# Kernel tuning notes

Measured on AMD Instinct MI355X. Metric: run time of the kernel, lower is better.

The kernel has to match this reference:

```python
import jax, jax.numpy as jnp
import numpy as np

N = 50000      # nodes
E = 800000     # edges (avg degree 16)
DIN = 128
DOUT = 128
L = 8          # num GCN2Conv layers
ALPHA = 0.1
THETA = 0.5


def setup_inputs() -> dict:
    key = jax.random.key(0)
    ks = jax.random.split(key, 5)
    x = jax.random.normal(ks[0], (N, DIN), jnp.float32)
    edge_index = jax.random.randint(ks[1], (2, E), 0, N, dtype=jnp.int64)
    # pre-normalized adjacency weights (normalize=False in GCN2Conv -> adj_t already normalized)
    edge_weight = jax.random.uniform(ks[2], (E,), jnp.float32) / 16.0
    W_lin = jax.random.normal(ks[3], (DIN, DOUT), jnp.float32) / np.sqrt(DIN).astype(np.float32)
    b_lin = jnp.zeros((DOUT,), jnp.float32)
    W_convs = jax.random.normal(ks[4], (L, DOUT, DOUT), jnp.float32) / np.sqrt(DOUT).astype(np.float32)
    return {"x": x, "edge_weight": edge_weight, "W_lin": W_lin, "b_lin": b_lin,
            "W_convs": W_convs, "edge_index": edge_index}


def reference(x, edge_weight, W_lin, b_lin, W_convs, edge_index):
    src, dst = edge_index[0], edge_index[1]
    # betas for GCN2Conv layer l (1-indexed): beta_l = log(theta/l + 1)
    betas = np.log(THETA / np.arange(1, L + 1) + 1.0).astype(np.float32)
    # x = lins(x).relu(); dropout p=0 is a no-op
    x0 = jax.nn.relu(x @ W_lin + b_lin)          # [N, DOUT]
    h = x0
    for l in range(L):
        # sparse propagate: agg = A @ h  (SpMM via gather + segment_sum)
        agg = jax.ops.segment_sum(h[src] * edge_weight[:, None], dst, num_segments=N)
        # initial-residual mixing
        m = (1.0 - ALPHA) * agg + ALPHA * x0
        # identity mapping (shared_weights): out = (1-beta)*m + beta*(m @ W)
        h = jax.nn.relu((1.0 - betas[l]) * m + betas[l] * (m @ W_convs[l]))
    return h
```

## Files before the change

### kernel.cpp

```cpp
#include <hip/hip_runtime.h>
#include <math.h>

#define N_NODES 50000
#define N_EDGES 800000
#define DIM 128
#define PAD 120

#define EPB 1024
#define NBLKA 782
#define BIN_SHIFT 8
#define NBIN 196
#define HISTW 197
#define PREP_BLOCKS 576

typedef __attribute__((ext_vector_type(8))) short short8;
typedef __attribute__((ext_vector_type(4))) float floatx4;

__device__ __forceinline__ unsigned short f32_to_bf16(float f) {
    unsigned int u = __float_as_uint(f);
    u += 0x7fffu + ((u >> 16) & 1u);
    return (unsigned short)(u >> 16);
}
__device__ __forceinline__ float bf16_to_f32(unsigned short h) {
    return __uint_as_float((unsigned int)h << 16);
}

__device__ __forceinline__ int swz(int row, int blk) {
    return row * 128 + (((blk ^ (row & 7)) & 15) << 3);
}

__global__ __launch_bounds__(256) void sortprep(const int* __restrict__ src,
                                                const int* __restrict__ dst,
                                                const float* __restrict__ ew,
                                                const float* __restrict__ Wlin,
                                                const float* __restrict__ Wcv,
                                                int* __restrict__ histg,
                                                int2* __restrict__ binbuf,
                                                unsigned short* __restrict__ WTg) {
    if (blockIdx.x >= NBLKA) {
        int i = (blockIdx.x - NBLKA) * 256 + threadIdx.x;
        int m = i >> 14;
        int n = (i >> 7) & 127;
        int k = i & 127;
        float v;
        if (m == 0) {
            v = Wlin[k * 128 + n];
        } else {
            int l = m - 1;
            float beta = logf(0.5f / (float)(l + 1) + 1.0f);
            v = beta * Wcv[(size_t)l * 16384 + k * 128 + n]
                + ((n == k) ? (1.0f - beta) : 0.0f);
        }
        WTg[i] = f32_to_bf16(v);
        return;
    }
    __shared__ int hist[NBIN];
    __shared__ int base[NBIN + 1];
    __shared__ int2 sorted[EPB];
    int tid = threadIdx.x;
    int e0 = blockIdx.x * EPB;
    int n = min(EPB, N_EDGES - e0);
    if (tid < NBIN) hist[tid] = 0;
    __syncthreads();
    for (int i = tid; i < n; i += 256) atomicAdd(&hist[dst[e0 + i] >> BIN_SHIFT], 1);
    __syncthreads();
    if (tid < NBIN) base[tid + 1] = hist[tid];
    if (tid == 0) base[0] = 0;
    __syncthreads();
    for (int off = 1; off < NBIN + 1; off <<= 1) {
        int v = 0;
        if (tid >= off && tid <= NBIN) v = base[tid - off];
        __syncthreads();
        if (tid >= off && tid <= NBIN) base[tid] += v;
        __syncthreads();
    }
    if (tid < NBIN) hist[tid] = base[tid];
    __syncthreads();
    for (int i = tid; i < n; i += 256) {
        int e = e0 + i;
        int d = dst[e];
        int pos = atomicAdd(&hist[d >> BIN_SHIFT], 1);
        int2 p;
        p.x = (src[e] & 0xFFFF) | (d << 16);
        p.y = __float_as_int(ew[e]);
        sorted[pos] = p;
    }
    __syncthreads();
    for (int k = tid; k < n; k += 256)
        binbuf[(size_t)blockIdx.x * EPB + k] = sorted[k];
    if (tid <= NBIN) histg[blockIdx.x * HISTW + tid] = base[tid];
}

__global__ __launch_bounds__(1024) void bin_scatter(const int* __restrict__ histg,
                                                    const int2* __restrict__ binbuf,
                                                    int* __restrict__ cnt,
                                                    int2* __restrict__ bucket) {
    __shared__ int c[256];
    int bin = blockIdx.x;
    int tid = threadIdx.x;
    if (tid < 256) c[tid] = 0;
    __syncthreads();
    if (tid < NBLKA) {
        int bs = histg[tid * HISTW + bin];
        int be = histg[tid * HISTW + bin + 1];
        const int2* sp = binbuf + (size_t)tid * EPB;
        for (int k = bs; k < be; k++) {
            int2 p = sp[k];
            int d = ((unsigned)p.x) >> 16;
            int pos = atomicAdd(&c[d & 255], 1);
            if (pos < PAD) {
                int2 q; q.x = p.x & 0xFFFF; q.y = p.y;
                bucket[(size_t)d * PAD + pos] = q;
            }
        }
    }
    __syncthreads();
    int node0 = bin << BIN_SHIFT;
    if (tid < 256 && node0 + tid < N_NODES)
        cnt[node0 + tid] = min(c[tid], PAD);
}

__global__ __launch_bounds__(256) void gemm_x0(const float* __restrict__ x,
                                               const unsigned short* __restrict__ WTg,
                                               const float* __restrict__ bias,
                                               unsigned short* __restrict__ x0B) {
    __shared__ unsigned short WT[128][136];
    for (int idx = threadIdx.x; idx < 2048; idx += 256) {
        int n = idx >> 4, c = idx & 15;
        *(short8*)(void*)&WT[n][c * 8] =
            *(const short8*)(const void*)(WTg + n * 128 + c * 8);
    }
    __syncthreads();
    int wave = threadIdx.x >> 6;
    int lane = threadIdx.x & 63;
    int r0 = (blockIdx.x * 4 + wave) * 16;
    if (r0 >= N_NODES) return;
    int mrow = lane & 15;
    int quad = lane >> 4;
    floatx4 acc[8];
#pragma unroll
    for (int t = 0; t < 8; t++) acc[t] = {0.f, 0.f, 0.f, 0.f};
#pragma unroll
    for (int k0 = 0; k0 < 128; k0 += 32) {
        const float* arow = x + (size_t)(r0 + mrow) * DIM;
        floatx4 alo = *(const floatx4*)(const void*)(arow + k0 + quad * 8);
        floatx4 ahi = *(const floatx4*)(const void*)(arow + k0 + quad * 8 + 4);
        short8 a;
#pragma unroll
        for (int j = 0; j < 4; j++) a[j] = (short)f32_to_bf16(alo[j]);
#pragma unroll
        for (int j = 0; j < 4; j++) a[4 + j] = (short)f32_to_bf16(ahi[j]);
#pragma unroll
        for (int t = 0; t < 8; t++) {
            short8 b = *(const short8*)(const void*)(&WT[t * 16 + mrow][k0 + quad * 8]);
            acc[t] = __builtin_amdgcn_mfma_f32_16x16x32_bf16(a, b, acc[t], 0, 0, 0);
        }
    }
#pragma unroll
    for (int t = 0; t < 8; t++) {
        int col = t * 16 + mrow;
        float bv = bias[col];
#pragma unroll
        for (int i = 0; i < 4; i++) {
            int row = r0 + quad * 4 + i;
            float v = fmaxf(acc[t][i] + bv, 0.f);
            x0B[(size_t)row * DIM + col] = f32_to_bf16(v);
        }
    }
}

__global__ __launch_bounds__(512, 4) void layer_fused(
        const unsigned short* __restrict__ hB,
        const unsigned short* __restrict__ x0B,
        const int* __restrict__ cnt,
        const int2* __restrict__ bucket,
        const unsigned short* __restrict__ WTg,
        float* __restrict__ outF,
        unsigned short* __restrict__ outB) {
    __shared__ unsigned short WT[128 * 128];
    __shared__ unsigned short M[32 * 128];
    int tid = threadIdx.x;
    for (int idx = tid; idx < 2048; idx += 512) {
        int n = idx >> 4, c = idx & 15;
        *(short8*)(void*)&WT[swz(n, c)] =
            *(const short8*)(const void*)(WTg + n * 128 + c * 8);
    }
    int wave = tid >> 6;
    int lane = tid & 63;
    int eg = lane >> 4;
    int fb = (lane & 15) * 8;
    int r0 = blockIdx.x * 32;

    for (int s = 0; s < 4; s++) {
        int row = (wave << 2) + s;
        int node = r0 + row;
        float acc[8] = {0.f, 0.f, 0.f, 0.f, 0.f, 0.f, 0.f, 0.f};
        if (node < N_NODES) {
            int end = min(cnt[node], PAD);
            if (end > 0) {
                const int2* ep = bucket + (size_t)node * PAD;
                int last = end - 1;
                for (int i = 0; i < end; i += 16) {
                    int i0 = i + eg, i1 = i0 + 4, i2 = i0 + 8, i3 = i0 + 12;
                    int2 e0 = ep[min(i0, last)];
                    int2 e1 = ep[min(i1, last)];
                    int2 e2 = ep[min(i2, last)];
                    int2 e3 = ep[min(i3, last)];
                    short8 r0v = *(const short8*)(const void*)(hB + (size_t)e0.x * DIM + fb);
                    short8 r1v = *(const short8*)(const void*)(hB + (size_t)e1.x * DIM + fb);
                    short8 r2v = *(const short8*)(const void*)(hB + (size_t)e2.x * DIM + fb);
                    short8 r3v = *(const short8*)(const void*)(hB + (size_t)e3.x * DIM + fb);
                    float w0 = (i0 < end) ? __int_as_float(e0.y) : 0.f;
                    float w1 = (i1 < end) ? __int_as_float(e1.y) : 0.f;
                    float w2 = (i2 < end) ? __int_as_float(e2.y) : 0.f;
                    float w3 = (i3 < end) ? __int_as_float(e3.y) : 0.f;
#pragma unroll
                    for (int j = 0; j < 8; j++) {
                        acc[j] = fmaf(w0, bf16_to_f32((unsigned short)r0v[j]), acc[j]);
                        acc[j] = fmaf(w1, bf16_to_f32((unsigned short)r1v[j]), acc[j]);
                        acc[j] = fmaf(w2, bf16_to_f32((unsigned short)r2v[j]), acc[j]);
                        acc[j] = fmaf(w3, bf16_to_f32((unsigned short)r3v[j]), acc[j]);
                    }
                }
            }
        }
#pragma unroll
        for (int j = 0; j < 8; j++) {
            acc[j] += __shfl_down(acc[j], 32);
            acc[j] += __shfl_down(acc[j], 16);
        }
        if (lane < 16) {
            short8 o;
            if (node < N_NODES) {
                short8 xv = *(const short8*)(const void*)(x0B + (size_t)node * DIM + fb);
#pragma unroll
                for (int j = 0; j < 8; j++)
                    o[j] = (short)f32_to_bf16(0.9f * acc[j]
                                              + 0.1f * bf16_to_f32((unsigned short)xv[j]));
            } else {
#pragma unroll
                for (int j = 0; j < 8; j++) o[j] = 0;
            }
            *(short8*)(void*)&M[swz(row, lane & 15)] = o;
        }
    }
    __syncthreads();

    int mrow = lane & 15;
    int quad = lane >> 4;
    int rt = wave >> 2;
    int ctb = (wave & 3) * 2;
    floatx4 acc2[2];
    acc2[0] = {0.f, 0.f, 0.f, 0.f};
    acc2[1] = {0.f, 0.f, 0.f, 0.f};
#pragma unroll
    for (int k0 = 0; k0 < 128; k0 += 32) {
        short8 a = *(const short8*)(const void*)(&M[swz(rt * 16 + mrow, k0 / 8 + quad)]);
#pragma unroll
        for (int t = 0; t < 2; t++) {
            short8 b = *(const short8*)(const void*)(&WT[swz((ctb + t) * 16 + mrow, k0 / 8 + quad)]);
            acc2[t] = __builtin_amdgcn_mfma_f32_16x16x32_bf16(a, b, acc2[t], 0, 0, 0);
        }
    }
#pragma unroll
    for (int t = 0; t < 2; t++) {
        int col = (ctb + t) * 16 + mrow;
#pragma unroll
        for (int i = 0; i < 4; i++) {
            int row = r0 + rt * 16 + quad * 4 + i;
            if (row < N_NODES) {
                float v = fmaxf(acc2[t][i], 0.f);
                size_t off = (size_t)row * DIM + col;
                if (outF) outF[off] = v;
                if (outB) outB[off] = f32_to_bf16(v);
            }
        }
    }
}


extern "C" void kernel_launch(void* const* d_in, const int* in_sizes, int n_in,
                              void* d_out, int out_size, void* d_ws, size_t ws_size,
                              hipStream_t stream) {
    const float* x    = (const float*)d_in[0];
    const float* ew   = (const float*)d_in[1];
    const float* Wlin = (const float*)d_in[2];
    const float* blin = (const float*)d_in[3];
    const float* Wcv  = (const float*)d_in[4];
    const int* eidx = (const int*)d_in[5];
    const int* esrc = eidx;
    const int* edst = eidx + N_EDGES;
    float* out = (float*)d_out;

    char* ws = (char*)d_ws;
    unsigned short* x0B = (unsigned short*)(ws);
    unsigned short* hA  = (unsigned short*)(ws + 12800000);
    unsigned short* hB2 = (unsigned short*)(ws + 25600000);
    int* cnt            = (int*)(ws + 38400000);
    int2* bucket        = (int2*)(ws + 38600064);
    unsigned short* WTg = (unsigned short*)(ws + 86600064);
    int* histg          = (int*)(ws + 86894976);
    int2* binbuf        = (int2*)ws;

    sortprep<<<NBLKA + PREP_BLOCKS, 256, 0, stream>>>(esrc, edst, ew, Wlin, Wcv,
                                                      histg, binbuf, WTg);

    bin_scatter<<<NBIN, 1024, 0, stream>>>(histg, binbuf, cnt, bucket);

    gemm_x0<<<(N_NODES + 63) / 64, 256, 0, stream>>>(x, WTg, blin, x0B);

    const unsigned short* hin = x0B;
    for (int l = 0; l < 8; l++) {
        unsigned short* hout = (l == 7) ? nullptr : ((l & 1) ? hB2 : hA);
        layer_fused<<<1563, 512, 0, stream>>>(hin, x0B, cnt, bucket,
                                              WTg + (size_t)(1 + l) * 16384,
                                              (l == 7) ? out : nullptr, hout);
        hin = hout;
    }
}
```

Measured before the change: 450.1 us.

## Fuse bin scatter and input GEMM into one heterogeneous kernel launch

```diff
diff --git a/kernel.cpp b/kernel.cpp
--- a/kernel.cpp
+++ b/kernel.cpp
@@ -12,6 +12,7 @@
 #define NBIN 196
 #define HISTW 197
 #define PREP_BLOCKS 576
+#define GEMM_BLOCKS 391
 
 typedef __attribute__((ext_vector_type(8))) short short8;
 typedef __attribute__((ext_vector_type(4))) float floatx4;
@@ -91,49 +92,50 @@
     if (tid <= NBIN) histg[blockIdx.x * HISTW + tid] = base[tid];
 }
 
-__global__ __launch_bounds__(1024) void bin_scatter(const int* __restrict__ histg,
-                                                    const int2* __restrict__ binbuf,
-                                                    int* __restrict__ cnt,
-                                                    int2* __restrict__ bucket) {
+__global__ __launch_bounds__(512) void fatB(const int* __restrict__ histg,
+                                            const int2* __restrict__ binbuf,
+                                            int* __restrict__ cnt,
+                                            int2* __restrict__ bucket,
+                                            const float* __restrict__ x,
+                                            const unsigned short* __restrict__ WTg,
+                                            const float* __restrict__ bias,
+                                            unsigned short* __restrict__ x0B) {
+    __shared__ unsigned short WT[128][136];
     __shared__ int c[256];
-    int bin = blockIdx.x;
     int tid = threadIdx.x;
-    if (tid < 256) c[tid] = 0;
-    __syncthreads();
-    if (tid < NBLKA) {
-        int bs = histg[tid * HISTW + bin];
-        int be = histg[tid * HISTW + bin + 1];
-        const int2* sp = binbuf + (size_t)tid * EPB;
-        for (int k = bs; k < be; k++) {
-            int2 p = sp[k];
-            int d = ((unsigned)p.x) >> 16;
-            int pos = atomicAdd(&c[d & 255], 1);
-            if (pos < PAD) {
-                int2 q; q.x = p.x & 0xFFFF; q.y = p.y;
-                bucket[(size_t)d * PAD + pos] = q;
+    if (blockIdx.x < NBIN) {
+        int bin = blockIdx.x;
+        if (tid < 256) c[tid] = 0;
+        __syncthreads();
+        for (int t = tid; t < NBLKA; t += 512) {
+            int bs = histg[t * HISTW + bin];
+            int be = histg[t * HISTW + bin + 1];
+            const int2* sp = binbuf + (size_t)t * EPB;
+            for (int k = bs; k < be; k++) {
+                int2 p = sp[k];
+                int d = ((unsigned)p.x) >> 16;
+                int pos = atomicAdd(&c[d & 255], 1);
+                if (pos < PAD) {
+                    int2 q; q.x = p.x & 0xFFFF; q.y = p.y;
+                    bucket[(size_t)d * PAD + pos] = q;
+                }
             }
         }
-    }
-    __syncthreads();
-    int node0 = bin << BIN_SHIFT;
-    if (tid < 256 && node0 + tid < N_NODES)
-        cnt[node0 + tid] = min(c[tid], PAD);
-}
-
-__global__ __launch_bounds__(256) void gemm_x0(const float* __restrict__ x,
-                                               const unsigned short* __restrict__ WTg,
-                                               const float* __restrict__ bias,
-                                               unsigned short* __restrict__ x0B) {
-    __shared__ unsigned short WT[128][136];
-    for (int idx = threadIdx.x; idx < 2048; idx += 256) {
-        int n = idx >> 4, c = idx & 15;
-        *(short8*)(void*)&WT[n][c * 8] =
-            *(const short8*)(const void*)(WTg + n * 128 + c * 8);
-    }
-    __syncthreads();
-    int wave = threadIdx.x >> 6;
-    int lane = threadIdx.x & 63;
-    int r0 = (blockIdx.x * 4 + wave) * 16;
+        __syncthreads();
+        int node0 = bin << BIN_SHIFT;
+        if (tid < 256 && node0 + tid < N_NODES)
+            cnt[node0 + tid] = min(c[tid], PAD);
+        return;
+    }
+    for (int idx = tid; idx < 2048; idx += 512) {
+        int n = idx >> 4, cc = idx & 15;
+        *(short8*)(void*)&WT[n][cc * 8] =
+            *(const short8*)(const void*)(WTg + n * 128 + cc * 8);
+    }
+    __syncthreads();
+    int wave = tid >> 6;
+    int lane = tid & 63;
+    int r0 = ((blockIdx.x - NBIN) * 8 + wave) * 16;
     if (r0 >= N_NODES) return;
     int mrow = lane & 15;
     int quad = lane >> 4;
@@ -300,14 +302,13 @@
     int2* bucket        = (int2*)(ws + 38600064);
     unsigned short* WTg = (unsigned short*)(ws + 86600064);
     int* histg          = (int*)(ws + 86894976);
-    int2* binbuf        = (int2*)ws;
+    int2* binbuf        = (int2*)hB2;
 
     sortprep<<<NBLKA + PREP_BLOCKS, 256, 0, stream>>>(esrc, edst, ew, Wlin, Wcv,
                                                       histg, binbuf, WTg);
 
-    bin_scatter<<<NBIN, 1024, 0, stream>>>(histg, binbuf, cnt, bucket);
-
-    gemm_x0<<<(N_NODES + 63) / 64, 256, 0, stream>>>(x, WTg, blin, x0B);
+    fatB<<<NBIN + GEMM_BLOCKS, 512, 0, stream>>>(histg, binbuf, cnt, bucket,
+                                                 x, WTg, blin, x0B);
 
     const unsigned short* hin = x0B;
     for (int l = 0; l < 8; l++) {
```

New measurement: 449.2 us, median of 2. Within noise of the previous version (-0.2%).
